# Kernel optimization log

Measured on AMD Instinct MI355X. Metric: run time of the kernel, lower is better.

Reference implementation:

```python
import math
import jax, jax.numpy as jnp
import numpy as np

B, T, C, NB = 2, 2048, 512, 4
EPS = 1.1920929e-7  # torch.finfo(float32).eps, used by F.rms_norm default


def rms_norm(x):
    return x * jax.lax.rsqrt(jnp.mean(x * x, axis=-1, keepdims=True) + EPS)


def rope(x):
    # standard rotary embedding over the last dim; x: (..., T, C)
    t_len, c = x.shape[-2], x.shape[-1]
    half = c // 2
    inv_freq = 1.0 / (10000.0 ** (jnp.arange(half, dtype=jnp.float32) / half))
    ang = jnp.arange(t_len, dtype=jnp.float32)[:, None] * inv_freq[None, :]  # (T, half)
    cos, sin = jnp.cos(ang), jnp.sin(ang)
    x1, x2 = x[..., :half], x[..., half:]
    return jnp.concatenate([x1 * cos - x2 * sin, x2 * cos + x1 * sin], axis=-1)


def setup_inputs() -> dict:
    key = jax.random.key(0)
    ks = jax.random.split(key, 8)
    sc = 1.0 / math.sqrt(C)
    return {
        "a": jax.random.normal(ks[0], (B, T, C), jnp.float32),
        "x": jax.random.normal(ks[1], (B, T, C), jnp.float32),
        "Wq": jax.random.normal(ks[2], (C, NB * C), jnp.float32) * sc,
        "Wk": jax.random.normal(ks[3], (C, C), jnp.float32) * sc,
        "Wv": jax.random.normal(ks[4], (C, NB * C), jnp.float32) * sc,
        "Wo": jax.random.normal(ks[5], (C, C), jnp.float32) * sc,
        "v_sink_residual": jax.random.normal(ks[6], (1, 1, 1, C), jnp.float32) * 0.02,
        "v_sink_basis": jax.random.normal(ks[7], (1, NB, 1, C), jnp.float32) * 0.02,
    }


def reference(a, x, Wq, Wk, Wv, Wo, v_sink_residual, v_sink_basis):
    # projections
    q = (a @ Wq).reshape(B, T, NB, C).transpose(0, 2, 1, 3)  # (B,NB,T,C)
    q = rms_norm(q)
    v = (a @ Wv).reshape(B, T, NB, C).transpose(0, 2, 1, 3)  # (B,NB,T,C)
    k = x @ Wk  # (B,T,C), single branch
    q, k = rope(q), rope(k)

    att = jnp.einsum('bntc,bsc->bnts', q, k) / math.sqrt(C)  # (B,NB,T,T)
    causal = jnp.tril(jnp.ones((T, T), dtype=bool))
    att = jnp.where(causal, att, -jnp.inf)

    # branch-axis softmax; fully-masked (non-causal) columns are all -inf -> nan -> 0
    m = jax.lax.stop_gradient(jnp.max(att, axis=1, keepdims=True))
    e = jnp.exp(att - m)
    soft_probs = jnp.nan_to_num(e / jnp.sum(e, axis=1, keepdims=True))

    # hard argmax routing with straight-through estimator
    max_val = jnp.max(soft_probs, axis=1, keepdims=True)
    hard_mask = (soft_probs == max_val).astype(soft_probs.dtype)
    route_mask = jax.lax.stop_gradient(hard_mask - soft_probs) + soft_probs  # (B,NB,T,T)

    # softplus gating on per-position max score
    scores_max = jnp.max(att, axis=1)          # (B,T,T)
    s = jax.nn.softplus(scores_max)            # softplus(-inf) = 0 on masked
    S = jnp.sum(s, axis=-1, keepdims=True)
    scale = jnp.minimum(1.0 / (S + 1e-6), 1.0)
    w = s * scale                              # (B,T,T)
    residual = 1.0 - jnp.sum(w, axis=-1, keepdims=True)  # (B,T,1)

    combined_weights = w[:, None] * route_mask           # (B,NB,T,T)
    y_context = jnp.einsum('bnts,bnsc->bntc', combined_weights, v)
    branch_activity = jnp.max(route_mask, axis=-1, keepdims=True)  # (B,NB,T,1)
    y_basis = branch_activity * v_sink_basis               # (B,NB,T,C)
    y_branches = jnp.sum(y_context + y_basis, axis=1)      # (B,T,C)
    y_res = residual * v_sink_residual[:, 0]               # (B,T,1)*(1,1,C) -> (B,T,C)
    y = y_branches + y_res
    return y @ Wo
```

## Files before the change

### kernel.cpp

```cpp
#include <hip/hip_runtime.h>
#include <math.h>

#define B_    2
#define T_    2048
#define C_    512
#define NB_   4
#define HALF_ 256
#define BT_   (B_*T_)
#define EPS_  1.1920929e-07f
#define RSC_  0.044194173824159216f

using f32x4 = __attribute__((ext_vector_type(4))) float;
using s16x8 = __attribute__((ext_vector_type(8))) short;
using u16x8 = __attribute__((ext_vector_type(8))) unsigned short;

__device__ __forceinline__ unsigned short f2bf(float f) {
    unsigned x = __float_as_uint(f);
    unsigned r = (x + 0x7fffu + ((x >> 16) & 1u)) >> 16;
    return (unsigned short)r;
}
__device__ __forceinline__ float bf2f(unsigned short h) {
    return __uint_as_float(((unsigned)h) << 16);
}

__device__ __forceinline__ void gl16(const void* g, void* l) {
    __builtin_amdgcn_global_load_lds(
        (const __attribute__((address_space(1))) unsigned int*)g,
        (__attribute__((address_space(3))) unsigned int*)l, 16, 0, 0);
}

__global__ __launch_bounds__(256) void rope_table_k(float* __restrict__ cosT,
                                                    float* __restrict__ sinT) {
    int t = blockIdx.x;
    int i = threadIdx.x;
    float ex   = (float)i / (float)HALF_;
    float invf = 1.0f / powf(10000.0f, ex);
    float ang  = (float)t * invf;
    float sv, cv;
    sincosf(ang, &sv, &cv);
    cosT[t*HALF_ + i] = cv;
    sinT[t*HALF_ + i] = sv;
}

__global__ __launch_bounds__(256) void cast2_hilo_k(const float* __restrict__ a,
                                                    const float* __restrict__ x,
                                                    unsigned short* __restrict__ ahi,
                                                    unsigned short* __restrict__ alo,
                                                    unsigned short* __restrict__ xhi,
                                                    unsigned short* __restrict__ xlo) {
    int i = blockIdx.x * 256 + threadIdx.x;
    const float* src; unsigned short *hi, *lo;
    if (i < 524288) { src = a; hi = ahi; lo = alo; }
    else { i -= 524288; src = x; hi = xhi; lo = xlo; }
    float4 v = ((const float4*)src)[i];
    ushort4 h, l;
    h.x = f2bf(v.x); l.x = f2bf(v.x - bf2f(h.x));
    h.y = f2bf(v.y); l.y = f2bf(v.y - bf2f(h.y));
    h.z = f2bf(v.z); l.z = f2bf(v.z - bf2f(h.z));
    h.w = f2bf(v.w); l.w = f2bf(v.w - bf2f(h.w));
    ((ushort4*)hi)[i] = h;
    ((ushort4*)lo)[i] = l;
}

__global__ __launch_bounds__(256) void tcast_k(const float* __restrict__ W,
                                               unsigned short* __restrict__ Whi,
                                               unsigned short* __restrict__ Wlo,
                                               int K, int N, int wantLo) {
    __shared__ float tile[64][65];
    int nbt = N >> 6;
    int nb = blockIdx.x % nbt, kb = blockIdx.x / nbt;
    int tid = threadIdx.x;
    int ty = tid >> 6, tx = tid & 63;
    for (int i = ty; i < 64; i += 4)
        tile[i][tx] = W[(size_t)(kb*64 + i) * N + nb*64 + tx];
    __syncthreads();
    for (int j = ty; j < 64; j += 4) {
        float v = tile[tx][j];
        unsigned short h = f2bf(v);
        size_t o = (size_t)(nb*64 + j) * K + kb*64 + tx;
        Whi[o] = h;
        if (wantLo) Wlo[o] = f2bf(v - bf2f(h));
    }
}

template<int SPLIT>
__global__ __launch_bounds__(256, 2) void mm_k(
    const unsigned short* __restrict__ Ahi, const unsigned short* __restrict__ Alo,
    const unsigned short* __restrict__ Bhi, const unsigned short* __restrict__ Blo,
    float* __restrict__ C, int M, int N, int K)
{
    constexpr int BUFS = SPLIT ? 16384 : 8192;
    __shared__ __align__(16) short smem[2 * BUFS];

    int tid = threadIdx.x;
    int w = tid >> 6, l = tid & 63;
    int wm = w >> 1, wn = w & 1;
    int llo = l & 15, lhi = l >> 4;
    int rs = tid >> 2, gs = tid & 3;
    int nwg = gridDim.x;
    int bid = blockIdx.x;
    int sb = (bid & 7) * (nwg >> 3) + (bid >> 3);
    int nbt = N >> 7;
    int bx = sb % nbt, by = sb / nbt;
    int m0 = by << 7, n0 = bx << 7;

    auto STAGE = [&](int cur, int k0) {
        short* base = smem + cur * BUFS;
        #pragma unroll
        for (int i8 = 0; i8 < 2; i8++) {
            int r = (i8 << 6) + rs;
            int fr = (r ^ (r >> 2)) & 3;
            int col = k0 + ((gs ^ fr) << 3);
            int db = ((i8 << 6) + (w << 4)) << 5;
            gl16(Ahi + (size_t)(m0 + r) * K + col, base + db);
            gl16(Bhi + (size_t)(n0 + r) * K + col, base + 4096 + db);
            if constexpr (SPLIT) {
                gl16(Alo + (size_t)(m0 + r) * K + col, base + 8192 + db);
                gl16(Blo + (size_t)(n0 + r) * K + col, base + 12288 + db);
            }
        }
    };

    f32x4 acc[4][4];
    #pragma unroll
    for (int mi = 0; mi < 4; mi++)
        #pragma unroll
        for (int ni = 0; ni < 4; ni++) acc[mi][ni] = (f32x4){0.f,0.f,0.f,0.f};

    const int NK = K >> 5;
    STAGE(0, 0);
    int cur = 0;
    for (int k = 0; k < NK; k++) {
        __syncthreads();
        if (k + 1 < NK) STAGE(cur ^ 1, (k + 1) << 5);
        short* Ah = smem + cur * BUFS;
        short* Bh = Ah + 4096;
        short* Al = Ah + 8192;
        short* Bl = Ah + 12288;
        s16x8 bh[4], bl[4];
        #pragma unroll
        for (int ni = 0; ni < 4; ni++) {
            int br = (wn << 6) + (ni << 4) + llo;
            int bo = (br << 5) + (((lhi ^ (br ^ (br >> 2))) & 3) << 3);
            bh[ni] = *(const s16x8*)&Bh[bo];
            if constexpr (SPLIT) bl[ni] = *(const s16x8*)&Bl[bo];
        }
        #pragma unroll
        for (int mi = 0; mi < 4; mi++) {
            int ar = (wm << 6) + (mi << 4) + llo;
            int ao = (ar << 5) + (((lhi ^ (ar ^ (ar >> 2))) & 3) << 3);
            s16x8 ah = *(const s16x8*)&Ah[ao];
            s16x8 al;
            if constexpr (SPLIT) al = *(const s16x8*)&Al[ao];
            #pragma unroll
            for (int ni = 0; ni < 4; ni++) {
                acc[mi][ni] = __builtin_amdgcn_mfma_f32_16x16x32_bf16(ah, bh[ni], acc[mi][ni], 0, 0, 0);
                if constexpr (SPLIT) {
                    acc[mi][ni] = __builtin_amdgcn_mfma_f32_16x16x32_bf16(ah, bl[ni], acc[mi][ni], 0, 0, 0);
                    acc[mi][ni] = __builtin_amdgcn_mfma_f32_16x16x32_bf16(al, bh[ni], acc[mi][ni], 0, 0, 0);
                }
            }
        }
        cur ^= 1;
    }
    #pragma unroll
    for (int mi = 0; mi < 4; mi++) {
        int row0 = m0 + (wm << 6) + (mi << 4) + (lhi << 2);
        #pragma unroll
        for (int ni = 0; ni < 4; ni++) {
            int col = n0 + (wn << 6) + (ni << 4) + llo;
            f32x4 v = acc[mi][ni];
            #pragma unroll
            for (int r = 0; r < 4; r++)
                C[(size_t)(row0 + r) * N + col] = v[r];
        }
    }
}

__global__ __launch_bounds__(256, 2) void mm_v_k(
    const unsigned short* __restrict__ Ahi,
    const unsigned short* __restrict__ Bhi,
    unsigned short* __restrict__ Vt, int M, int N, int K)
{
    __shared__ __align__(16) short smem[2 * 8192];
    int tid = threadIdx.x;
    int w = tid >> 6, l = tid & 63;
    int wm = w >> 1, wn = w & 1;
    int llo = l & 15, lhi = l >> 4;
    int rs = tid >> 2, gs = tid & 3;
    int nwg = gridDim.x;
    int bid = blockIdx.x;
    int sb = (bid & 7) * (nwg >> 3) + (bid >> 3);
    int nbt = N >> 7;
    int bx = sb % nbt, by = sb / nbt;
    int m0 = by << 7, n0 = bx << 7;

    auto STAGE = [&](int cur, int k0) {
        short* base = smem + cur * 8192;
        #pragma unroll
        for (int i8 = 0; i8 < 2; i8++) {
            int r = (i8 << 6) + rs;
            int fr = (r ^ (r >> 2)) & 3;
            int col = k0 + ((gs ^ fr) << 3);
            int db = ((i8 << 6) + (w << 4)) << 5;
            gl16(Ahi + (size_t)(m0 + r) * K + col, base + db);
            gl16(Bhi + (size_t)(n0 + r) * K + col, base + 4096 + db);
        }
    };

    f32x4 acc[4][4];
    #pragma unroll
    for (int mi = 0; mi < 4; mi++)
        #pragma unroll
        for (int ni = 0; ni < 4; ni++) acc[mi][ni] = (f32x4){0.f,0.f,0.f,0.f};

    const int NK = K >> 5;
    STAGE(0, 0);
    int cur = 0;
    for (int k = 0; k < NK; k++) {
        __syncthreads();
        if (k + 1 < NK) STAGE(cur ^ 1, (k + 1) << 5);
        short* Ah = smem + cur * 8192;
        short* Bh = Ah + 4096;
        s16x8 bh[4];
        #pragma unroll
        for (int ni = 0; ni < 4; ni++) {
            int br = (wn << 6) + (ni << 4) + llo;
            bh[ni] = *(const s16x8*)&Bh[(br << 5) + (((lhi ^ (br ^ (br >> 2))) & 3) << 3)];
        }
        #pragma unroll
        for (int mi = 0; mi < 4; mi++) {
            int ar = (wm << 6) + (mi << 4) + llo;
            s16x8 ah = *(const s16x8*)&Ah[(ar << 5) + (((lhi ^ (ar ^ (ar >> 2))) & 3) << 3)];
            #pragma unroll
            for (int ni = 0; ni < 4; ni++)
                acc[mi][ni] = __builtin_amdgcn_mfma_f32_16x16x32_bf16(ah, bh[ni], acc[mi][ni], 0, 0, 0);
        }
        cur ^= 1;
    }
    #pragma unroll
    for (int mi = 0; mi < 4; mi++) {
        int row0 = m0 + (wm << 6) + (mi << 4) + (lhi << 2);
        int b = row0 >> 11, t = row0 & (T_ - 1);
        #pragma unroll
        for (int ni = 0; ni < 4; ni++) {
            int col = n0 + (wn << 6) + (ni << 4) + llo;
            f32x4 v = acc[mi][ni];
            ushort4 o;
            o.x = f2bf(v[0]); o.y = f2bf(v[1]); o.z = f2bf(v[2]); o.w = f2bf(v[3]);
            *(ushort4*)(Vt + ((size_t)(b*(NB_*C_) + col)) * T_ + t) = o;
        }
    }
}

__global__ __launch_bounds__(256) void q_post3_k(const float* __restrict__ Qf,
                                                 const float* __restrict__ cosT,
                                                 const float* __restrict__ sinT,
                                                 unsigned short* __restrict__ Qhi,
                                                 unsigned short* __restrict__ Qlo) {
    int bt = blockIdx.x;
    int t  = bt & (T_ - 1);
    int w = threadIdx.x >> 6, l = threadIdx.x & 63;
    const float* row = Qf + (size_t)bt * (NB_*C_) + (w << 9);
    int i0 = l << 2;
    float4 x1 = *(const float4*)(row + i0);
    float4 x2 = *(const float4*)(row + i0 + HALF_);
    float s = x1.x*x1.x + x1.y*x1.y + x1.z*x1.z + x1.w*x1.w
            + x2.x*x2.x + x2.y*x2.y + x2.z*x2.z + x2.w*x2.w;
    #pragma unroll
    for (int mask = 1; mask <= 32; mask <<= 1) s += __shfl_xor(s, mask, 64);
    float r = rsqrtf(s * (1.0f / (float)C_) + EPS_);
    float4 cv = *(const float4*)(cosT + t*HALF_ + i0);
    float4 sv = *(const float4*)(sinT + t*HALF_ + i0);
    float v1[4], v2[4];
    v1[0] = x1.x*r*cv.x - x2.x*r*sv.x;  v2[0] = x2.x*r*cv.x + x1.x*r*sv.x;
    v1[1] = x1.y*r*cv.y - x2.y*r*sv.y;  v2[1] = x2.y*r*cv.y + x1.y*r*sv.y;
    v1[2] = x1.z*r*cv.z - x2.z*r*sv.z;  v2[2] = x2.z*r*cv.z + x1.z*r*sv.z;
    v1[3] = x1.w*r*cv.w - x2.w*r*sv.w;  v2[3] = x2.w*r*cv.w + x1.w*r*sv.w;
    size_t o = (size_t)bt * (NB_*C_) + (w << 9) + i0;
    ushort4 h1, h2, l1, l2;
    h1.x = f2bf(v1[0]); l1.x = f2bf(v1[0] - bf2f(h1.x));
    h1.y = f2bf(v1[1]); l1.y = f2bf(v1[1] - bf2f(h1.y));
    h1.z = f2bf(v1[2]); l1.z = f2bf(v1[2] - bf2f(h1.z));
    h1.w = f2bf(v1[3]); l1.w = f2bf(v1[3] - bf2f(h1.w));
    h2.x = f2bf(v2[0]); l2.x = f2bf(v2[0] - bf2f(h2.x));
    h2.y = f2bf(v2[1]); l2.y = f2bf(v2[1] - bf2f(h2.y));
    h2.z = f2bf(v2[2]); l2.z = f2bf(v2[2] - bf2f(h2.z));
    h2.w = f2bf(v2[3]); l2.w = f2bf(v2[3] - bf2f(h2.w));
    *(ushort4*)(Qhi + o)          = h1;
    *(ushort4*)(Qhi + o + HALF_)  = h2;
    *(ushort4*)(Qlo + o)          = l1;
    *(ushort4*)(Qlo + o + HALF_)  = l2;
}

__global__ __launch_bounds__(256) void k_post3_k(const float* __restrict__ Kf,
                                                 const float* __restrict__ cosT,
                                                 const float* __restrict__ sinT,
                                                 unsigned short* __restrict__ Khi,
                                                 unsigned short* __restrict__ Klo) {
    int sub = threadIdx.x >> 7, l = threadIdx.x & 127;
    int bt = blockIdx.x * 2 + sub;
    int t  = bt & (T_ - 1);
    const float* row = Kf + (size_t)bt * C_;
    int i0 = l << 1;
    float2 x1 = *(const float2*)(row + i0);
    float2 x2 = *(const float2*)(row + i0 + HALF_);
    float2 cv = *(const float2*)(cosT + t*HALF_ + i0);
    float2 sv = *(const float2*)(sinT + t*HALF_ + i0);
    float v1x = x1.x*cv.x - x2.x*sv.x, v2x = x2.x*cv.x + x1.x*sv.x;
    float v1y = x1.y*cv.y - x2.y*sv.y, v2y = x2.y*cv.y + x1.y*sv.y;
    size_t o = (size_t)bt * C_ + i0;
    ushort2 h1, h2, l1, l2;
    h1.x = f2bf(v1x); l1.x = f2bf(v1x - bf2f(h1.x));
    h1.y = f2bf(v1y); l1.y = f2bf(v1y - bf2f(h1.y));
    h2.x = f2bf(v2x); l2.x = f2bf(v2x - bf2f(h2.x));
    h2.y = f2bf(v2y); l2.y = f2bf(v2y - bf2f(h2.y));
    *(ushort2*)(Khi + o)         = h1;
    *(ushort2*)(Khi + o + HALF_) = h2;
    *(ushort2*)(Klo + o)         = l1;
    *(ushort2*)(Klo + o + HALF_) = l2;
}

__global__ __launch_bounds__(256, 2) void qk_routing_k(
    const unsigned short* __restrict__ Qhi, const unsigned short* __restrict__ Qlo,
    const unsigned short* __restrict__ Khi, const unsigned short* __restrict__ Klo,
    unsigned short* __restrict__ P, float* __restrict__ partS, unsigned* __restrict__ partA)
{
    __shared__ __align__(16) short smem[32768];

    int tid = threadIdx.x;
    int w = tid >> 6, l = tid & 63;
    int wm = w >> 1, wn = w & 1;
    int llo = l & 15, lhi = l >> 4;
    int rs = tid >> 2, gs = tid & 3;

    int bid = blockIdx.x;
    int j = (bid & 7) * 136 + (bid >> 3);
    int b = (j >= 544) ? 1 : 0;
    int j2 = j - 544 * b;
    int q = (int)((sqrtf(1.0f + 2.0f*(float)j2) - 1.0f) * 0.5f);
    if (2*(q+1)*(q+2) <= j2) q++;
    if (2*q*(q+1) > j2) q--;
    int r0 = j2 - 2*q*(q+1);
    int tloc = r0 / (q+1);
    int st = r0 - tloc*(q+1);
    int tt = (q << 2) + tloc;
    int t0 = tt << 5, s0 = st << 7;

    auto STAGE = [&](int cur, int k0) {
        short* base = smem + (cur << 14);
        #pragma unroll
        for (int i8 = 0; i8 < 2; i8++) {
            int r = (i8 << 6) + rs;
            int fr = (r ^ (r >> 2)) & 3;
            int col = k0 + ((gs ^ fr) << 3);
            int db = ((i8 << 6) + (w << 4)) << 5;
            size_t ga = (size_t)(b*T_ + t0 + (r >> 2)) * (NB_*C_) + ((r & 3) << 9) + col;
            size_t gb = (size_t)(b*T_ + s0 + r) * C_ + col;
            gl16(Qhi + ga, base + db);
            gl16(Khi + gb, base + 4096 + db);
            gl16(Qlo + ga, base + 8192 + db);
            gl16(Klo + gb, base + 12288 + db);
        }
    };

    f32x4 acc[4][4];
    #pragma unroll
    for (int mi = 0; mi < 4; mi++)
        #pragma unroll
        for (int ni = 0; ni < 4; ni++) acc[mi][ni] = (f32x4){0.f,0.f,0.f,0.f};

    STAGE(0, 0);
    int cur = 0;
    for (int k = 0; k < 16; k++) {
        __syncthreads();
        if (k < 15) STAGE(cur ^ 1, (k + 1) << 5);
        short* Ah = smem + (cur << 14);
        short* Bh = Ah + 4096;
        short* Al = Ah + 8192;
        short* Bl = Ah + 12288;
        s16x8 bh[4], bl[4];
        #pragma unroll
        for (int ni = 0; ni < 4; ni++) {
            int br = (wn << 6) + (ni << 4) + llo;
            int bo = (br << 5) + (((lhi ^ (br ^ (br >> 2))) & 3) << 3);
            bh[ni] = *(const s16x8*)&Bh[bo];
            bl[ni] = *(const s16x8*)&Bl[bo];
        }
        #pragma unroll
        for (int mi = 0; mi < 4; mi++) {
            int ar = (wm << 6) + (mi << 4) + llo;
            int ao = (ar << 5) + (((lhi ^ (ar ^ (ar >> 2))) & 3) << 3);
            s16x8 ah = *(const s16x8*)&Ah[ao];
            s16x8 al = *(const s16x8*)&Al[ao];
            #pragma unroll
            for (int ni = 0; ni < 4; ni++) {
                acc[mi][ni] = __builtin_amdgcn_mfma_f32_16x16x32_bf16(ah, bh[ni], acc[mi][ni], 0, 0, 0);
                acc[mi][ni] = __builtin_amdgcn_mfma_f32_16x16x32_bf16(ah, bl[ni], acc[mi][ni], 0, 0, 0);
                acc[mi][ni] = __builtin_amdgcn_mfma_f32_16x16x32_bf16(al, bh[ni], acc[mi][ni], 0, 0, 0);
            }
        }
        cur ^= 1;
    }
    __syncthreads();

    short* Pl = smem;
    #pragma unroll
    for (int mi = 0; mi < 4; mi++) {
        int tl = (wm << 4) + (mi << 2) + lhi;
        int tg = t0 + tl;
        float wsum = 0.f; unsigned ab = 0u;
        #pragma unroll
        for (int ni = 0; ni < 4; ni++) {
            int sl = (wn << 6) + (ni << 4) + llo;
            int sg = s0 + sl;
            f32x4 v = acc[mi][ni];
            float wu = 0.f; unsigned bits = 0u;
            if (sg <= tg) {
                float a0 = v[0]*RSC_, a1 = v[1]*RSC_, a2 = v[2]*RSC_, a3 = v[3]*RSC_;
                float m = fmaxf(fmaxf(a0, a1), fmaxf(a2, a3));
                bits = (a0 == m ? 1u : 0u) | (a1 == m ? 2u : 0u)
                     | (a2 == m ? 4u : 0u) | (a3 == m ? 8u : 0u);
                wu = fmaxf(m, 0.f) + log1pf(expf(-fabsf(m)));
                wsum += wu; ab |= bits;
            }
            unsigned short wub = f2bf(wu);
            Pl[(0*32 + tl)*136 + sl] = (bits & 1u) ? (short)wub : (short)0;
            Pl[(1*32 + tl)*136 + sl] = (bits & 2u) ? (short)wub : (short)0;
            Pl[(2*32 + tl)*136 + sl] = (bits & 4u) ? (short)wub : (short)0;
            Pl[(3*32 + tl)*136 + sl] = (bits & 8u) ? (short)wub : (short)0;
        }
        #pragma unroll
        for (int mask = 1; mask <= 8; mask <<= 1) wsum += __shfl_xor(wsum, mask, 64);
        int ai = (int)ab;
        #pragma unroll
        for (int mask = 1; mask <= 8; mask <<= 1) ai |= __shfl_xor(ai, mask, 64);
        if (llo == 0) {
            size_t pidx = ((((size_t)(b*64 + tt) * 16 + st) * 2 + wn) * 32) + tl;
            partS[pidx] = wsum;
            partA[pidx] = (unsigned)ai;
        }
    }
    __syncthreads();
    for (int i = tid; i < 2048; i += 256) {
        int row = i >> 4, g8 = i & 15;
        int n = row >> 5, tl = row & 31;
        u16x8 v = *(const u16x8*)&Pl[row*136 + (g8 << 3)];
        *(u16x8*)(P + ((size_t)((b*4 + n)*T_ + t0 + tl)) * T_ + s0 + (g8 << 3)) = v;
    }
}

__global__ __launch_bounds__(256, 2) void pv_k(
    const unsigned short* __restrict__ P, const unsigned short* __restrict__ Vt,
    float* __restrict__ py)
{
    __shared__ __align__(16) short smem[32768];
    int tid = threadIdx.x;
    int w = tid >> 6, l = tid & 63;
    int wm = w >> 1, wn = w & 1;
    int llo = l & 15, lhi = l >> 4;
    int rl = l >> 3, gs8 = l & 7;
    int rb = w << 5;
    int bid = blockIdx.x;
    int ph = bid & 3, cc = (bid >> 2) & 3, tt = 15 - ((bid >> 4) & 15), b = bid >> 8;
    int t0 = tt << 7, c0 = cc << 7;
    int b4 = b * 4;
    size_t bV = (size_t)b * (NB_*C_);

    auto STAGE = [&](int cur, int n, int k0) {
        short* base = smem + (cur << 14);
        #pragma unroll
        for (int i8 = 0; i8 < 4; i8++) {
            int r = rb + (i8 << 3) + rl;
            int sg = (gs8 ^ (r & 7)) << 3;
            int dsb = (rb + (i8 << 3)) << 6;
            gl16(P  + ((size_t)((b4 + n)*T_ + t0 + r)) * T_ + k0 + sg, base + dsb);
            gl16(Vt + (bV + (size_t)((n << 9) + c0 + r)) * T_ + k0 + sg, base + 8192 + dsb);
        }
    };

    f32x4 acc[4][4];
    #pragma unroll
    for (int mi = 0; mi < 4; mi++)
        #pragma unroll
        for (int ni = 0; ni < 4; ni++) acc[mi][ni] = (f32x4){0.f,0.f,0.f,0.f};

    int first_sb = ph << 7;
    int num_sb = (first_sb <= t0 + 127) ? (((t0 + 127 - first_sb) >> 9) + 1) : 0;
    int nsteps = num_sb << 3;

    if (nsteps > 0) {
        int n_p = 0, sb_p = first_sb, h_p = 0;
        auto ADV = [&]() {
            h_p ^= 1;
            if (!h_p) { sb_p += 512; if (sb_p > t0 + 127) { sb_p = first_sb; n_p++; } }
        };
        STAGE(0, n_p, sb_p + (h_p << 6)); ADV();
        int cur = 0;
        for (int s = 0; s < nsteps; s++) {
            __syncthreads();
            if (s + 1 < nsteps) { STAGE(cur ^ 1, n_p, sb_p + (h_p << 6)); ADV(); }
            short* Ah = smem + (cur << 14);
            short* Bh = Ah + 8192;
            #pragma unroll
            for (int ks = 0; ks < 2; ks++) {
                s16x8 bh[4];
                #pragma unroll
                for (int ni = 0; ni < 4; ni++) {
                    int br = (wn << 6) + (ni << 4) + llo;
                    bh[ni] = *(const s16x8*)&Bh[br*64 + ((((ks << 2) + lhi) ^ (br & 7)) << 3)];
                }
                #pragma unroll
                for (int mi = 0; mi < 4; mi++) {
                    int ar = (wm << 6) + (mi << 4) + llo;
                    s16x8 ah = *(const s16x8*)&Ah[ar*64 + ((((ks << 2) + lhi) ^ (ar & 7)) << 3)];
                    #pragma unroll
                    for (int ni = 0; ni < 4; ni++)
                        acc[mi][ni] = __builtin_amdgcn_mfma_f32_16x16x32_bf16(ah, bh[ni], acc[mi][ni], 0, 0, 0);
                }
            }
            cur ^= 1;
        }
    }
    float* out = py + (size_t)ph * (BT_*(size_t)C_);
    #pragma unroll
    for (int mi = 0; mi < 4; mi++) {
        int row0 = t0 + (wm << 6) + (mi << 4) + (lhi << 2);
        #pragma unroll
        for (int ni = 0; ni < 4; ni++) {
            int col = c0 + (wn << 6) + (ni << 4) + llo;
            f32x4 v = acc[mi][ni];
            #pragma unroll
            for (int r = 0; r < 4; r++)
                out[(size_t)(b*T_ + row0 + r) * C_ + col] = v[r];
        }
    }
}

__global__ __launch_bounds__(256) void combine3_k(
    const float* __restrict__ py, const float* __restrict__ partS,
    const unsigned* __restrict__ partA,
    const float* __restrict__ basis, const float* __restrict__ resid_sink,
    unsigned short* __restrict__ ybf)
{
    int bt = blockIdx.x;
    int t = bt & (T_ - 1);
    int b = bt >> 11;
    int i = threadIdx.x;
    int tt32 = t >> 5, tl = t & 31;
    int stmax = tt32 >> 2;
    float S = 0.f; unsigned act = 0u;
    for (int st = 0; st <= stmax; st++) {
        #pragma unroll
        for (int wn = 0; wn < 2; wn++) {
            size_t idx = ((((size_t)(b*64 + tt32) * 16 + st) * 2 + wn) * 32) + tl;
            S += partS[idx];
            act |= partA[idx];
        }
    }
    float y0 = 0.f, y1 = 0.f;
    #pragma unroll
    for (int ph = 0; ph < 4; ph++) {
        y0 += py[(size_t)ph * (BT_*(size_t)C_) + (size_t)bt * C_ + i];
        y1 += py[(size_t)ph * (BT_*(size_t)C_) + (size_t)bt * C_ + i + 256];
    }
    float scale = fminf(1.0f / (S + 1e-6f), 1.0f);
    float residual = 1.0f - scale * S;
    if (t < T_ - 1) act = 0xFu;
    float o0 = scale * y0, o1 = scale * y1;
    #pragma unroll
    for (int n = 0; n < 4; n++) if ((act >> n) & 1u) {
        o0 += basis[n*C_ + i];
        o1 += basis[n*C_ + i + 256];
    }
    o0 += residual * resid_sink[i];
    o1 += residual * resid_sink[i + 256];
    ybf[(size_t)bt * C_ + i]       = f2bf(o0);
    ybf[(size_t)bt * C_ + i + 256] = f2bf(o1);
}

extern "C" void kernel_launch(void* const* d_in, const int* in_sizes, int n_in,
                              void* d_out, int out_size, void* d_ws, size_t ws_size,
                              hipStream_t stream) {
    const float* a    = (const float*)d_in[0];
    const float* x    = (const float*)d_in[1];
    const float* Wq   = (const float*)d_in[2];
    const float* Wk   = (const float*)d_in[3];
    const float* Wv   = (const float*)d_in[4];
    const float* Wo   = (const float*)d_in[5];
    const float* vres = (const float*)d_in[6];
    const float* vbas = (const float*)d_in[7];

    float* ws = (float*)d_ws;
    float* cosT = ws;
    float* sinT = cosT + 524288;
    float* Qf   = sinT + 524288;
    float* Kf   = Qf + 8388608;
    unsigned short* ahi  = (unsigned short*)(Kf + 2097152);
    unsigned short* alo  = ahi  + 2097152;
    unsigned short* xhi  = alo  + 2097152;
    unsigned short* xlo  = xhi  + 2097152;
    unsigned short* Wqth = xlo  + 2097152;
    unsigned short* Wqtl = Wqth + 1048576;
    unsigned short* Wkth = Wqtl + 1048576;
    unsigned short* Wktl = Wkth + 262144;
    unsigned short* Wvth = Wktl + 262144;
    unsigned short* Woth = Wvth + 1048576;
    unsigned short* Qhi  = Woth + 262144;
    unsigned short* Qlo  = Qhi  + 8388608;
    unsigned short* Khi  = Qlo  + 8388608;
    unsigned short* Klo  = Khi  + 2097152;
    unsigned short* Vt   = Klo  + 2097152;
    unsigned short* P    = Vt   + 8388608;

    float* py = Qf;
    float* partS = Kf;
    unsigned* partA = (unsigned*)(Kf + 131072);
    unsigned short* ybf = (unsigned short*)(Kf + 262144);

    rope_table_k<<<T_, 256, 0, stream>>>(cosT, sinT);
    cast2_hilo_k<<<4096, 256, 0, stream>>>(a, x, ahi, alo, xhi, xlo);
    tcast_k<<<256, 256, 0, stream>>>(Wq, Wqth, Wqtl, 512, 2048, 1);
    tcast_k<<<64,  256, 0, stream>>>(Wk, Wkth, Wktl, 512, 512,  1);
    tcast_k<<<256, 256, 0, stream>>>(Wv, Wvth, nullptr, 512, 2048, 0);
    tcast_k<<<64,  256, 0, stream>>>(Wo, Woth, nullptr, 512, 512,  0);

    mm_k<1><<<512, 256, 0, stream>>>(ahi, alo, Wqth, Wqtl, Qf, BT_, 2048, 512);
    mm_k<1><<<128, 256, 0, stream>>>(xhi, xlo, Wkth, Wktl, Kf, BT_, 512, 512);
    mm_v_k<<<512, 256, 0, stream>>>(ahi, Wvth, Vt, BT_, 2048, 512);

    q_post3_k<<<BT_, 256, 0, stream>>>(Qf, cosT, sinT, Qhi, Qlo);
    k_post3_k<<<BT_/2, 256, 0, stream>>>(Kf, cosT, sinT, Khi, Klo);

    qk_routing_k<<<1088, 256, 0, stream>>>(Qhi, Qlo, Khi, Klo, P, partS, partA);
    pv_k<<<512, 256, 0, stream>>>(P, Vt, py);
    combine3_k<<<BT_, 256, 0, stream>>>(py, partS, partA, vbas, vres, ybf);

    mm_k<0><<<128, 256, 0, stream>>>(ybf, nullptr, Woth, nullptr, (float*)d_out, BT_, 512, 512);
}
```

Before: 243.4 us.

## Overlap global-to-LDS prefetch with compute via explicit waitcnt barriers; bf16 partial outputs

The GEMM-style kernels (projection, QK, PV) now issue the next stage's global-to-LDS loads before waiting, then use explicit vmcnt waits and raw barriers instead of __syncthreads at loop top. This lets the prefetch overlap the current tile's MFMA work. Per-thread address offsets are hoisted out of the staging lambda, and launch bounds allow more waves per CU for non-split GEMMs. PV partial outputs are stored as bf16 instead of fp32, which halves that traffic but adds rounding error to the summed context.

```diff
diff --git a/kernel.cpp b/kernel.cpp
--- a/kernel.cpp
+++ b/kernel.cpp
@@ -28,6 +28,17 @@
         (const __attribute__((address_space(1))) unsigned int*)g,
         (__attribute__((address_space(3))) unsigned int*)l, 16, 0, 0);
 }
+
+template<int N> __device__ __forceinline__ void wait_vm() {
+    if constexpr (N == 0)      asm volatile("s_waitcnt vmcnt(0)" ::: "memory");
+    else if constexpr (N == 4) asm volatile("s_waitcnt vmcnt(4)" ::: "memory");
+    else                       asm volatile("s_waitcnt vmcnt(8)" ::: "memory");
+}
+__device__ __forceinline__ void wait_lgkm0() {
+    asm volatile("s_waitcnt lgkmcnt(0)" ::: "memory");
+}
+__device__ __forceinline__ void bar() { __builtin_amdgcn_s_barrier(); }
+__device__ __forceinline__ void sbar0() { __builtin_amdgcn_sched_barrier(0); }
 
 __global__ __launch_bounds__(256) void rope_table_k(float* __restrict__ cosT,
                                                     float* __restrict__ sinT) {
@@ -84,12 +95,13 @@
 }
 
 template<int SPLIT>
-__global__ __launch_bounds__(256, 2) void mm_k(
+__global__ __launch_bounds__(256, SPLIT ? 2 : 4) void mm_k(
     const unsigned short* __restrict__ Ahi, const unsigned short* __restrict__ Alo,
     const unsigned short* __restrict__ Bhi, const unsigned short* __restrict__ Blo,
     float* __restrict__ C, int M, int N, int K)
 {
     constexpr int BUFS = SPLIT ? 16384 : 8192;
+    constexpr int L = SPLIT ? 8 : 4;
     __shared__ __align__(16) short smem[2 * BUFS];
 
     int tid = threadIdx.x;
@@ -104,19 +116,27 @@
     int bx = sb % nbt, by = sb / nbt;
     int m0 = by << 7, n0 = bx << 7;
 
+    size_t ga[2], gb[2];
+    int db_[2];
+    #pragma unroll
+    for (int i8 = 0; i8 < 2; i8++) {
+        int r = (i8 << 6) + rs;
+        int fr = (r ^ (r >> 2)) & 3;
+        int col = (gs ^ fr) << 3;
+        ga[i8] = (size_t)(m0 + r) * K + col;
+        gb[i8] = (size_t)(n0 + r) * K + col;
+        db_[i8] = ((i8 << 6) + (w << 4)) << 5;
+    }
+
     auto STAGE = [&](int cur, int k0) {
         short* base = smem + cur * BUFS;
         #pragma unroll
         for (int i8 = 0; i8 < 2; i8++) {
-            int r = (i8 << 6) + rs;
-            int fr = (r ^ (r >> 2)) & 3;
-            int col = k0 + ((gs ^ fr) << 3);
-            int db = ((i8 << 6) + (w << 4)) << 5;
-            gl16(Ahi + (size_t)(m0 + r) * K + col, base + db);
-            gl16(Bhi + (size_t)(n0 + r) * K + col, base + 4096 + db);
+            gl16(Ahi + ga[i8] + k0, base + db_[i8]);
+            gl16(Bhi + gb[i8] + k0, base + 4096 + db_[i8]);
             if constexpr (SPLIT) {
-                gl16(Alo + (size_t)(m0 + r) * K + col, base + 8192 + db);
-                gl16(Blo + (size_t)(n0 + r) * K + col, base + 12288 + db);
+                gl16(Alo + ga[i8] + k0, base + 8192 + db_[i8]);
+                gl16(Blo + gb[i8] + k0, base + 12288 + db_[i8]);
             }
         }
     };
@@ -131,8 +151,9 @@
     STAGE(0, 0);
     int cur = 0;
     for (int k = 0; k < NK; k++) {
-        __syncthreads();
-        if (k + 1 < NK) STAGE(cur ^ 1, (k + 1) << 5);
+        if (k + 1 < NK) { STAGE(cur ^ 1, (k + 1) << 5); wait_vm<L>(); }
+        else wait_vm<0>();
+        bar(); sbar0();
         short* Ah = smem + cur * BUFS;
         short* Bh = Ah + 4096;
         short* Al = Ah + 8192;
@@ -161,6 +182,7 @@
                 }
             }
         }
+        wait_lgkm0(); sbar0(); bar();
         cur ^= 1;
     }
     #pragma unroll
@@ -177,7 +199,7 @@
     }
 }
 
-__global__ __launch_bounds__(256, 2) void mm_v_k(
+__global__ __launch_bounds__(256, 4) void mm_v_k(
     const unsigned short* __restrict__ Ahi,
     const unsigned short* __restrict__ Bhi,
     unsigned short* __restrict__ Vt, int M, int N, int K)
@@ -195,16 +217,23 @@
     int bx = sb % nbt, by = sb / nbt;
     int m0 = by << 7, n0 = bx << 7;
 
+    size_t ga[2], gb[2];
+    int db_[2];
+    #pragma unroll
+    for (int i8 = 0; i8 < 2; i8++) {
+        int r = (i8 << 6) + rs;
+        int fr = (r ^ (r >> 2)) & 3;
+        int col = (gs ^ fr) << 3;
+        ga[i8] = (size_t)(m0 + r) * K + col;
+        gb[i8] = (size_t)(n0 + r) * K + col;
+        db_[i8] = ((i8 << 6) + (w << 4)) << 5;
+    }
     auto STAGE = [&](int cur, int k0) {
         short* base = smem + cur * 8192;
         #pragma unroll
         for (int i8 = 0; i8 < 2; i8++) {
-            int r = (i8 << 6) + rs;
-            int fr = (r ^ (r >> 2)) & 3;
-            int col = k0 + ((gs ^ fr) << 3);
-            int db = ((i8 << 6) + (w << 4)) << 5;
-            gl16(Ahi + (size_t)(m0 + r) * K + col, base + db);
-            gl16(Bhi + (size_t)(n0 + r) * K + col, base + 4096 + db);
+            gl16(Ahi + ga[i8] + k0, base + db_[i8]);
+            gl16(Bhi + gb[i8] + k0, base + 4096 + db_[i8]);
         }
     };
 
@@ -218,8 +247,9 @@
     STAGE(0, 0);
     int cur = 0;
     for (int k = 0; k < NK; k++) {
-        __syncthreads();
-        if (k + 1 < NK) STAGE(cur ^ 1, (k + 1) << 5);
+        if (k + 1 < NK) { STAGE(cur ^ 1, (k + 1) << 5); wait_vm<4>(); }
+        else wait_vm<0>();
+        bar(); sbar0();
         short* Ah = smem + cur * 8192;
         short* Bh = Ah + 4096;
         s16x8 bh[4];
@@ -236,6 +266,7 @@
             for (int ni = 0; ni < 4; ni++)
                 acc[mi][ni] = __builtin_amdgcn_mfma_f32_16x16x32_bf16(ah, bh[ni], acc[mi][ni], 0, 0, 0);
         }
+        wait_lgkm0(); sbar0(); bar();
         cur ^= 1;
     }
     #pragma unroll
@@ -347,20 +378,25 @@
     int tt = (q << 2) + tloc;
     int t0 = tt << 5, s0 = st << 7;
 
+    size_t ga[2], gb[2];
+    int db_[2];
+    #pragma unroll
+    for (int i8 = 0; i8 < 2; i8++) {
+        int r = (i8 << 6) + rs;
+        int fr = (r ^ (r >> 2)) & 3;
+        int col = (gs ^ fr) << 3;
+        ga[i8] = (size_t)(b*T_ + t0 + (r >> 2)) * (NB_*C_) + ((r & 3) << 9) + col;
+        gb[i8] = (size_t)(b*T_ + s0 + r) * C_ + col;
+        db_[i8] = ((i8 << 6) + (w << 4)) << 5;
+    }
     auto STAGE = [&](int cur, int k0) {
         short* base = smem + (cur << 14);
         #pragma unroll
         for (int i8 = 0; i8 < 2; i8++) {
-            int r = (i8 << 6) + rs;
-            int fr = (r ^ (r >> 2)) & 3;
-            int col = k0 + ((gs ^ fr) << 3);
-            int db = ((i8 << 6) + (w << 4)) << 5;
-            size_t ga = (size_t)(b*T_ + t0 + (r >> 2)) * (NB_*C_) + ((r & 3) << 9) + col;
-            size_t gb = (size_t)(b*T_ + s0 + r) * C_ + col;
-            gl16(Qhi + ga, base + db);
-            gl16(Khi + gb, base + 4096 + db);
-            gl16(Qlo + ga, base + 8192 + db);
-            gl16(Klo + gb, base + 12288 + db);
+            gl16(Qhi + ga[i8] + k0, base + db_[i8]);
+            gl16(Khi + gb[i8] + k0, base + 4096 + db_[i8]);
+            gl16(Qlo + ga[i8] + k0, base + 8192 + db_[i8]);
+            gl16(Klo + gb[i8] + k0, base + 12288 + db_[i8]);
         }
     };
 
@@ -373,8 +409,9 @@
     STAGE(0, 0);
     int cur = 0;
     for (int k = 0; k < 16; k++) {
-        __syncthreads();
-        if (k < 15) STAGE(cur ^ 1, (k + 1) << 5);
+        if (k + 1 < 16) { STAGE(cur ^ 1, (k + 1) << 5); wait_vm<8>(); }
+        else wait_vm<0>();
+        bar(); sbar0();
         short* Ah = smem + (cur << 14);
         short* Bh = Ah + 4096;
         short* Al = Ah + 8192;
@@ -400,6 +437,7 @@
                 acc[mi][ni] = __builtin_amdgcn_mfma_f32_16x16x32_bf16(al, bh[ni], acc[mi][ni], 0, 0, 0);
             }
         }
+        wait_lgkm0(); sbar0(); bar();
         cur ^= 1;
     }
     __syncthreads();
@@ -452,7 +490,7 @@
 
 __global__ __launch_bounds__(256, 2) void pv_k(
     const unsigned short* __restrict__ P, const unsigned short* __restrict__ Vt,
-    float* __restrict__ py)
+    unsigned short* __restrict__ py)
 {
     __shared__ __align__(16) short smem[32768];
     int tid = threadIdx.x;
@@ -467,15 +505,24 @@
     int b4 = b * 4;
     size_t bV = (size_t)b * (NB_*C_);
 
+    size_t pa_[4], pb_[4];
+    int dsb_[4];
+    #pragma unroll
+    for (int i8 = 0; i8 < 4; i8++) {
+        int r = rb + (i8 << 3) + rl;
+        int sg = (gs8 ^ (r & 7)) << 3;
+        pa_[i8] = (size_t)(t0 + r) * T_ + sg;
+        pb_[i8] = (size_t)(c0 + r) * T_ + sg;
+        dsb_[i8] = (rb + (i8 << 3)) << 6;
+    }
     auto STAGE = [&](int cur, int n, int k0) {
         short* base = smem + (cur << 14);
+        size_t na = (size_t)(b4 + n) * T_ * T_;
+        size_t nb = (bV + (size_t)(n << 9)) * T_;
         #pragma unroll
         for (int i8 = 0; i8 < 4; i8++) {
-            int r = rb + (i8 << 3) + rl;
-            int sg = (gs8 ^ (r & 7)) << 3;
-            int dsb = (rb + (i8 << 3)) << 6;
-            gl16(P  + ((size_t)((b4 + n)*T_ + t0 + r)) * T_ + k0 + sg, base + dsb);
-            gl16(Vt + (bV + (size_t)((n << 9) + c0 + r)) * T_ + k0 + sg, base + 8192 + dsb);
+            gl16(P  + na + pa_[i8] + k0, base + dsb_[i8]);
+            gl16(Vt + nb + pb_[i8] + k0, base + 8192 + dsb_[i8]);
         }
     };
 
@@ -498,8 +545,9 @@
         STAGE(0, n_p, sb_p + (h_p << 6)); ADV();
         int cur = 0;
         for (int s = 0; s < nsteps; s++) {
-            __syncthreads();
-            if (s + 1 < nsteps) { STAGE(cur ^ 1, n_p, sb_p + (h_p << 6)); ADV(); }
+            if (s + 1 < nsteps) { STAGE(cur ^ 1, n_p, sb_p + (h_p << 6)); ADV(); wait_vm<8>(); }
+            else wait_vm<0>();
+            bar(); sbar0();
             short* Ah = smem + (cur << 14);
             short* Bh = Ah + 8192;
             #pragma unroll
@@ -519,10 +567,11 @@
                         acc[mi][ni] = __builtin_amdgcn_mfma_f32_16x16x32_bf16(ah, bh[ni], acc[mi][ni], 0, 0, 0);
                 }
             }
+            wait_lgkm0(); sbar0(); bar();
             cur ^= 1;
         }
     }
-    float* out = py + (size_t)ph * (BT_*(size_t)C_);
+    unsigned short* out = py + (size_t)ph * (BT_*(size_t)C_);
     #pragma unroll
     for (int mi = 0; mi < 4; mi++) {
         int row0 = t0 + (wm << 6) + (mi << 4) + (lhi << 2);
@@ -532,13 +581,13 @@
             f32x4 v = acc[mi][ni];
             #pragma unroll
             for (int r = 0; r < 4; r++)
-                out[(size_t)(b*T_ + row0 + r) * C_ + col] = v[r];
+                out[(size_t)(b*T_ + row0 + r) * C_ + col] = f2bf(v[r]);
         }
     }
 }
 
 __global__ __launch_bounds__(256) void combine3_k(
-    const float* __restrict__ py, const float* __restrict__ partS,
+    const unsigned short* __restrict__ py, const float* __restrict__ partS,
     const unsigned* __restrict__ partA,
     const float* __restrict__ basis, const float* __restrict__ resid_sink,
     unsigned short* __restrict__ ybf)
@@ -561,8 +610,8 @@
     float y0 = 0.f, y1 = 0.f;
     #pragma unroll
     for (int ph = 0; ph < 4; ph++) {
-        y0 += py[(size_t)ph * (BT_*(size_t)C_) + (size_t)bt * C_ + i];
-        y1 += py[(size_t)ph * (BT_*(size_t)C_) + (size_t)bt * C_ + i + 256];
+        y0 += bf2f(py[(size_t)ph * (BT_*(size_t)C_) + (size_t)bt * C_ + i]);
+        y1 += bf2f(py[(size_t)ph * (BT_*(size_t)C_) + (size_t)bt * C_ + i + 256]);
     }
     float scale = fminf(1.0f / (S + 1e-6f), 1.0f);
     float residual = 1.0f - scale * S;
@@ -613,7 +662,7 @@
     unsigned short* Vt   = Klo  + 2097152;
     unsigned short* P    = Vt   + 8388608;
 
-    float* py = Qf;
+    unsigned short* py = (unsigned short*)Qf;
     float* partS = Kf;
     unsigned* partA = (unsigned*)(Kf + 131072);
     unsigned short* ybf = (unsigned short*)(Kf + 262144);
```

Result: no change. 243.6 us (+0.1%).
